# Kernel tuning notes

Measured on AMD Instinct MI355X. Metric: run time of the kernel, lower is better.

The kernel has to match this reference:

```python
import jax, jax.numpy as jnp
import numpy as np

D = 128           # embed_dim
NUM_LAYERS = 2
N_CLASSES = 4
OUT_CELL = 64
SPEAKERS = 2
INPUT_DIMS = [768, 74, 35]
B, T = 32, 60


def setup_inputs() -> dict:
    key = jax.random.key(0)
    ks = jax.random.split(key, 24)
    inp = {}
    inp['x0'] = jax.random.normal(ks[0], (B, T, INPUT_DIMS[0]), jnp.float32)
    inp['x1'] = jax.random.normal(ks[1], (B, T, INPUT_DIMS[1]), jnp.float32)
    inp['x2'] = jax.random.normal(ks[2], (B, T, INPUT_DIMS[2]), jnp.float32)
    inp['smask'] = jax.random.normal(ks[3], (B, T, SPEAKERS), jnp.float32)  # argmax -> speaker ids
    # modality projections
    for i, d in enumerate(INPUT_DIMS):
        inp[f'Wp{i}'] = jax.random.normal(ks[4 + i], (d, D), jnp.float32) / np.float32(np.sqrt(d))
        inp[f'bp{i}'] = jnp.zeros((D,), jnp.float32)
    # shared PositionEmbedding (ModuleList([m]*3) shares params)
    inp['freq_emb'] = jax.random.normal(ks[7], (SPEAKERS, D), jnp.float32) * 0.1
    inp['phase_emb'] = jax.random.normal(ks[8], (SPEAKERS, D), jnp.float32)
    # shared QRNNCell (ModuleList([cell]*num_layers) shares params)
    inp['U_x'] = jnp.linalg.qr(jax.random.normal(ks[9], (D, D), jnp.float32))[0]
    inp['U_h'] = jnp.linalg.qr(jax.random.normal(ks[10], (D, D), jnp.float32))[0]
    inp['Lambda'] = jnp.float32(0.5)
    # QMeasurement kernel (real/imag parts of D measurement vectors)
    inp['kernel_r'] = jnp.eye(D, dtype=jnp.float32) + 0.05 * jax.random.normal(ks[11], (D, D), jnp.float32)
    inp['kernel_i'] = 0.05 * jax.random.normal(ks[12], (D, D), jnp.float32)
    # SimpleNet fc_out
    inp['W1'] = jax.random.normal(ks[13], (D, OUT_CELL), jnp.float32) / np.float32(np.sqrt(D))
    inp['b1'] = jnp.zeros((OUT_CELL,), jnp.float32)
    inp['W2'] = jax.random.normal(ks[14], (OUT_CELL, N_CLASSES), jnp.float32) / np.float32(np.sqrt(OUT_CELL))
    inp['b2'] = jnp.zeros((N_CLASSES,), jnp.float32)
    return inp


def _qmn_forward(x0, x1, x2, smask, Wp0, bp0, Wp1, bp1, Wp2, bp2,
                 freq_emb, phase_emb, U_x, U_h, Lambda,
                 kernel_r, kernel_i, W1, b1, W2, b2):
    xs = [x0, x1, x2]
    Ws = [(Wp0, bp0), (Wp1, bp1), (Wp2, bp2)]
    reps = [jax.nn.relu(x @ W + b) for x, (W, b) in zip(xs, Ws)]           # [B,T,D] each
    # mixture weights: softmax over per-modality L2 norms
    norms = jnp.concatenate([jnp.linalg.norm(r, axis=-1, keepdims=True) for r in reps], axis=-1)
    weights = jax.nn.softmax(norms, axis=-1)                               # [B,T,M]
    # shared phase embedding: phase = t * freq[speaker] + phase[speaker]
    ids = jnp.argmax(smask, axis=-1)                                       # [B,T] int
    pos = jnp.arange(T, dtype=jnp.float32)[None, :, None]                  # [1,T,1]
    phase = pos * freq_emb[ids] + phase_emb[ids]                           # [B,T,D]
    cosp, sinp = jnp.cos(phase), jnp.sin(phase)
    # mixed density matrices rho = sum_m w_m |v_m><v_m|
    rho_r = jnp.zeros((B, T, D, D), jnp.float32)
    rho_i = jnp.zeros((B, T, D, D), jnp.float32)
    for m, r in enumerate(reps):
        a = r / jnp.maximum(jnp.linalg.norm(r, axis=-1, keepdims=True), 1e-12)
        pr = a * cosp                                                       # real amplitude
        pi = a * sinp                                                       # imag amplitude
        w = weights[..., m][..., None, None]
        rho_r = rho_r + w * (jnp.einsum('btm,btn->btmn', pr, pr) + jnp.einsum('btm,btn->btmn', pi, pi))
        rho_i = rho_i + w * (jnp.einsum('btm,btn->btmn', pi, pr) - jnp.einsum('btm,btn->btmn', pr, pi))
    # time-major for scan
    sr = jnp.transpose(rho_r, (1, 0, 2, 3))                                # [T,B,D,D]
    si = jnp.transpose(rho_i, (1, 0, 2, 3))

    def cell(h, x):
        hr, hi = h
        xr, xi = x
        Xr = jnp.einsum('mp,bpq,nq->bmn', U_x, xr, U_x)
        Xi = jnp.einsum('mp,bpq,nq->bmn', U_x, xi, U_x)
        Hr = jnp.einsum('mp,bpq,nq->bmn', U_h, hr, U_h)
        Hi = jnp.einsum('mp,bpq,nq->bmn', U_h, hi, U_h)
        nr = Lambda * Hr + (1.0 - Lambda) * Xr
        ni = Lambda * Hi + (1.0 - Lambda) * Xi
        return (nr, ni), (nr, ni)

    h0 = (jnp.broadcast_to(jnp.eye(D, dtype=jnp.float32) / D, (B, D, D)),
          jnp.zeros((B, D, D), jnp.float32))
    for _ in range(NUM_LAYERS):  # same shared cell params each layer
        _, (sr, si) = jax.lax.scan(cell, h0, (sr, si))
    # QMeasurement: p_k = Re(v_k^dag rho v_k), unit-norm complex measurement vectors
    nrm = jnp.sqrt(jnp.sum(kernel_r**2 + kernel_i**2, axis=1, keepdims=True))
    vr = kernel_r / jnp.maximum(nrm, 1e-12)                                # [K,D], K=D
    vi = kernel_i / jnp.maximum(nrm, 1e-12)
    probs = (jnp.einsum('tbmn,km,kn->tbk', sr, vr, vr)
             + jnp.einsum('tbmn,km,kn->tbk', sr, vi, vi)
             - jnp.einsum('tbmn,km,kn->tbk', si, vr, vi)
             + jnp.einsum('tbmn,km,kn->tbk', si, vi, vr))                  # [T,B,D]
    # SimpleNet (dropout = identity at inference)
    hid = jax.nn.relu(probs @ W1 + b1)
    out = jnp.tanh(hid @ W2 + b2)                                          # [T,B,C]
    out = jnp.transpose(out, (1, 0, 2))                                    # [B,T,C]
    return jax.nn.log_softmax(out, axis=2)


def reference(x0, x1, x2, smask, Wp0, bp0, Wp1, bp1, Wp2, bp2,
              freq_emb, phase_emb, U_x, U_h, Lambda,
              kernel_r, kernel_i, W1, b1, W2, b2):
    return _qmn_forward(x0, x1, x2, smask, Wp0, bp0, Wp1, bp1, Wp2, bp2,
                        freq_emb, phase_emb, U_x, U_h, Lambda,
                        kernel_r, kernel_i, W1, b1, W2, b2)
```

## Files before the change

### kernel.cpp

```cpp
#include <hip/hip_runtime.h>


#define DB 32
#define DT 60
#define DD 128
#define BT (DB*DT)
#define SP 136

typedef unsigned short ushort_t;
typedef __attribute__((ext_vector_type(8))) __bf16 bf16x8;
typedef __attribute__((ext_vector_type(8))) unsigned short ushort8_t;
typedef __attribute__((ext_vector_type(4))) float  float4v;

__device__ __forceinline__ float bf2f(ushort_t u){
  union { unsigned int i; float f; } x; x.i = ((unsigned int)u) << 16; return x.f;
}
__device__ __forceinline__ ushort_t f2bf(float f){
  union { float f; unsigned int i; } x; x.f = f;
  unsigned int lsb = (x.i >> 16) & 1u;
  return (ushort_t)((x.i + 0x7FFFu + lsb) >> 16);
}
__device__ __forceinline__ unsigned int f2bfpk(float a, float b){
#if defined(__gfx950__) && __has_builtin(__builtin_amdgcn_cvt_pk_bf16_f32)
  auto v = __builtin_amdgcn_cvt_pk_bf16_f32(a, b);
  unsigned int r; __builtin_memcpy(&r, &v, 4); return r;
#else
  return (unsigned int)f2bf(a) | ((unsigned int)f2bf(b) << 16);
#endif
}
__device__ __forceinline__ void split2(float v, ushort_t& h, ushort_t& l){
  h = f2bf(v); l = f2bf(v - bf2f(h));
}

template<int RT, int CT, bool ALO, bool BLO>
__device__ __forceinline__ void gemm_t(const ushort_t* Ah, const ushort_t* Al,
                                       const ushort_t* Bh, const ushort_t* Bl,
                                       float4v* acc, int row0, int col0, int gma, int q)
{
  for (int ks = 0; ks < 4; ks++){
    int ko = ks*32 + q*8;
    bf16x8 aF[RT], aL[RT], bF[CT], bL[CT];
    #pragma unroll
    for (int R = 0; R < RT; R++){
      int row = row0 + 16*R + gma;
      aF[R] = *(const bf16x8*)&Ah[row*SP + ko];
      if (ALO) aL[R] = *(const bf16x8*)&Al[row*SP + ko];
    }
    #pragma unroll
    for (int C = 0; C < CT; C++){
      int row = col0 + 16*C + gma;
      bF[C] = *(const bf16x8*)&Bh[row*SP + ko];
      if (BLO) bL[C] = *(const bf16x8*)&Bl[row*SP + ko];
    }
    #pragma unroll
    for (int R = 0; R < RT; R++)
      #pragma unroll
      for (int C = 0; C < CT; C++){
        float4v c = acc[R*CT+C];
        c = __builtin_amdgcn_mfma_f32_16x16x32_bf16(aF[R], bF[C], c, 0, 0, 0);
        if (BLO) c = __builtin_amdgcn_mfma_f32_16x16x32_bf16(aF[R], bL[C], c, 0, 0, 0);
        if (ALO) c = __builtin_amdgcn_mfma_f32_16x16x32_bf16(aL[R], bF[C], c, 0, 0, 0);
        acc[R*CT+C] = c;
      }
  }
}

template<int RT, int CT>
__device__ __forceinline__ void emit_t(const float4v* acc, ushort_t* dst, int stride,
                                       int row0, int col0, int gma, int q){
  #pragma unroll
  for (int R = 0; R < RT; R++)
    #pragma unroll
    for (int C = 0; C < CT; C++){
      int c = col0 + 16*C + gma, r0 = row0 + 16*R + 4*q;
      uint2 o;
      o.x = f2bfpk(acc[R*CT+C][0], acc[R*CT+C][1]);
      o.y = f2bfpk(acc[R*CT+C][2], acc[R*CT+C][3]);
      *(uint2*)&dst[(size_t)c*stride + r0] = o;
    }
}
template<int RT, int CT>
__device__ __forceinline__ void emit_split_t(const float4v* acc, ushort_t* dh, ushort_t* dl, int stride,
                                             int row0, int col0, int gma, int q){
  #pragma unroll
  for (int R = 0; R < RT; R++)
    #pragma unroll
    for (int C = 0; C < CT; C++){
      int c = col0 + 16*C + gma, r0 = row0 + 16*R + 4*q;
      ushort4 hh, ll;
      split2(acc[R*CT+C][0], hh.x, ll.x); split2(acc[R*CT+C][1], hh.y, ll.y);
      split2(acc[R*CT+C][2], hh.z, ll.z); split2(acc[R*CT+C][3], hh.w, ll.w);
      *(ushort4*)&dh[(size_t)c*stride + r0] = hh;
      *(ushort4*)&dl[(size_t)c*stride + r0] = ll;
    }
}
template<int NT>
__device__ __forceinline__ void lds_load_mat(ushort_t* dst, const ushort_t* src, int tid){
  for (int i = tid*8; i < 16384; i += NT*8){
    int r = i >> 7, k = i & 127;
    *(ushort8_t*)&dst[r*SP + k] = *(const ushort8_t*)&src[i];
  }
}
template<int NT>
__device__ __forceinline__ void lds_load_rows16(ushort_t* dst, const ushort_t* src, int tid){
  for (int i = tid*8; i < 2048; i += NT*8){
    int r = i >> 7, k = i & 127;
    *(ushort8_t*)&dst[r*SP + k] = *(const ushort8_t*)&src[i];
  }
}
template<int NT>
__device__ __forceinline__ void lds_load_mat2(ushort_t* d0, const ushort_t* s0,
                                              ushort_t* d1, const ushort_t* s1, int tid){
  constexpr int CH = 16384/(NT*8);
  ushort8_t r0[CH], r1[CH];
  #pragma unroll
  for (int c = 0; c < CH; c++) r0[c] = *(const ushort8_t*)&s0[tid*8 + c*NT*8];
  #pragma unroll
  for (int c = 0; c < CH; c++) r1[c] = *(const ushort8_t*)&s1[tid*8 + c*NT*8];
  #pragma unroll
  for (int c = 0; c < CH; c++){
    int i = tid*8 + c*NT*8; int r = i >> 7, k = i & 127;
    *(ushort8_t*)&d0[r*SP + k] = r0[c];
  }
  #pragma unroll
  for (int c = 0; c < CH; c++){
    int i = tid*8 + c*NT*8; int r = i >> 7, k = i & 127;
    *(ushort8_t*)&d1[r*SP + k] = r1[c];
  }
}
template<int NT>
__device__ __forceinline__ void lds_store_mat(ushort_t* dst, const ushort_t* src, int tid){
  for (int i = tid*8; i < 16384; i += NT*8){
    int r = i >> 7, k = i & 127;
    *(ushort8_t*)&dst[i] = *(const ushort8_t*)&src[r*SP + k];
  }
}

__global__ void k_small(const float* Ux, const float* Uh, const float* kr, const float* ki,
                        const float* Wp0, const float* Wp1, const float* Wp2,
                        const float* x0, const float* x1, const float* x2,
                        ushort_t* UxTh, ushort_t* UxTl, ushort_t* UxH, ushort_t* UxL,
                        float* Vr, float* Vi,
                        ushort_t* PpH, ushort_t* PpL, ushort_t* PTh, ushort_t* PTl,
                        ushort_t* WT0h, ushort_t* WT0l, ushort_t* WT1h, ushort_t* WT1l,
                        ushort_t* WT2h, ushort_t* WT2l,
                        ushort_t* X0h, ushort_t* X0l, ushort_t* X1h, ushort_t* X1l,
                        ushort_t* X2h, ushort_t* X2l){
  int blk = blockIdx.x, d = threadIdx.x;
  if (blk < 128){
    int i = blk;
    float v = Ux[i*DD + d];
    ushort_t h, l; split2(v, h, l);
    UxTh[d*DD + i] = h; UxTl[d*DD + i] = l;
  } else if (blk < 256){
    __shared__ float red[DD];
    int k = blk - 128;
    float r = kr[k*DD+d], im = ki[k*DD+d];
    red[d] = r*r + im*im;
    __syncthreads();
    for (int s = 64; s > 0; s >>= 1){ if (d < s) red[d] += red[d+s]; __syncthreads(); }
    float nrm = fmaxf(sqrtf(red[0]), 1e-12f);
    Vr[k*DD+d] = r/nrm; Vi[k*DD+d] = im/nrm;
  } else if (blk < 384){
    int i = blk - 256;
    float v = Uh[i*DD + d];
    ushort_t h, l; split2(v, h, l);
    PpH[i*DD + d] = h;  PpL[i*DD + d] = l;
    PTh[d*DD + i] = h;  PTl[d*DD + i] = l;
  } else if (blk < 512){
    int dd2 = blk - 384;
    ushort_t h, l;
    for (int k = d; k < 768; k += 128){
      split2(Wp0[(size_t)k*DD + dd2], h, l);
      WT0h[(size_t)dd2*768 + k] = h; WT0l[(size_t)dd2*768 + k] = l;
    }
    { float v = (d < 74) ? Wp1[(size_t)d*DD + dd2] : 0.f;
      split2(v, h, l); WT1h[dd2*128 + d] = h; WT1l[dd2*128 + d] = l; }
    { float v = (d < 35) ? Wp2[(size_t)d*DD + dd2] : 0.f;
      split2(v, h, l); WT2h[dd2*128 + d] = h; WT2l[dd2*128 + d] = l; }
    { split2(Ux[(size_t)dd2*DD + d], h, l);
      UxH[dd2*DD + d] = h; UxL[dd2*DD + d] = l; }
  } else {
    int bt = blk - 512;
    ushort_t h, l;
    const float* r0 = x0 + (size_t)bt*768;
    #pragma unroll
    for (int j = 0; j < 6; j++){
      split2(r0[j*128 + d], h, l);
      X0h[(size_t)bt*768 + j*128 + d] = h;
      X0l[(size_t)bt*768 + j*128 + d] = l;
    }
    float v1 = (d < 74) ? x1[(size_t)bt*74 + d] : 0.f;
    split2(v1, h, l);
    X1h[(size_t)bt*128 + d] = h; X1l[(size_t)bt*128 + d] = l;
    float v2 = (d < 35) ? x2[(size_t)bt*35 + d] : 0.f;
    split2(v2, h, l);
    X2h[(size_t)bt*128 + d] = h; X2l[(size_t)bt*128 + d] = l;
  }
}

__global__ __launch_bounds__(512,1) void k_proj(
    const ushort_t* X0h, const ushort_t* X0l, const ushort_t* X1h, const ushort_t* X1l,
    const ushort_t* X2h, const ushort_t* X2l,
    const ushort_t* WT0h, const ushort_t* WT0l, const ushort_t* WT1h, const ushort_t* WT1l,
    const ushort_t* WT2h, const ushort_t* WT2l,
    const float* bp1, const float* bp2,
    float* Rpart, float* Reps)
{
  __shared__ ushort_t Ah[128*SP], Al[128*SP], Bh[128*SP], Bl[128*SP];
  int blk = blockIdx.x;
  int m, tile, ch;
  if (blk < 90){ m = 0; tile = blk/6; ch = blk%6; }
  else if (blk < 105){ m = 1; tile = blk-90; ch = 0; }
  else { m = 2; tile = blk-105; ch = 0; }
  int bt0 = tile*128;
  int tid = threadIdx.x;
  int w = tid >> 6, lane = tid & 63, gma = lane & 15, q = lane >> 4;
  int row0 = 32*(w >> 1), col0 = 64*(w & 1);
  const ushort_t* Wh_ = (m==0)? WT0h : (m==1)? WT1h : WT2h;
  const ushort_t* Wl_ = (m==0)? WT0l : (m==1)? WT1l : WT2l;
  const ushort_t* Xh_ = (m==0)? X0h : (m==1)? X1h : X2h;
  const ushort_t* Xl_ = (m==0)? X0l : (m==1)? X1l : X2l;
  int KX = (m==0)? 768 : 128;
  for (int i = tid*8; i < 16384; i += 4096){
    int r = i >> 7, k = i & 127;
    *(ushort8_t*)&Ah[r*SP + k] = *(const ushort8_t*)&Wh_[(size_t)r*KX + ch*128 + k];
    *(ushort8_t*)&Al[r*SP + k] = *(const ushort8_t*)&Wl_[(size_t)r*KX + ch*128 + k];
    *(ushort8_t*)&Bh[r*SP + k] = *(const ushort8_t*)&Xh_[(size_t)(bt0+r)*KX + ch*128 + k];
    *(ushort8_t*)&Bl[r*SP + k] = *(const ushort8_t*)&Xl_[(size_t)(bt0+r)*KX + ch*128 + k];
  }
  __syncthreads();
  float4v acc[8];
  #pragma unroll
  for (int i = 0; i < 8; i++) acc[i] = (float4v){0.f,0.f,0.f,0.f};
  gemm_t<2,4,true,true>(Ah, Al, Bh, Bl, acc, row0, col0, gma, q);
  if (m == 0){
    #pragma unroll
    for (int R = 0; R < 2; R++)
      #pragma unroll
      for (int C = 0; C < 4; C++){
        int c = col0 + 16*C + gma, r0 = row0 + 16*R + 4*q;
        float4 o;
        o.x = acc[R*4+C][0]; o.y = acc[R*4+C][1];
        o.z = acc[R*4+C][2]; o.w = acc[R*4+C][3];
        *(float4*)&Rpart[((size_t)ch*BT + bt0 + c)*128 + r0] = o;
      }
  } else {
    const float* bp = (m==1)? bp1 : bp2;
    #pragma unroll
    for (int R = 0; R < 2; R++){
      int r0 = row0 + 16*R + 4*q;
      float4 bv = *(const float4*)&bp[r0];
      #pragma unroll
      for (int C = 0; C < 4; C++){
        int c = col0 + 16*C + gma;
        float4v a = acc[R*4+C];
        float4 o;
        o.x = fmaxf(a[0]+bv.x, 0.f); o.y = fmaxf(a[1]+bv.y, 0.f);
        o.z = fmaxf(a[2]+bv.z, 0.f); o.w = fmaxf(a[3]+bv.w, 0.f);
        *(float4*)&Reps[(size_t)(bt0 + c)*384 + m*128 + r0] = o;
      }
    }
  }
}

__global__ __launch_bounds__(128) void k_mix(const float* Rpart, const float* Reps,
    const float* bp0, const float* smask,
    const float* freq, const float* phem, ushort_t* PsH, ushort_t* PsL, float* Wgt)
{
  __shared__ float part[2][3];
  int bt = blockIdx.x; int t = bt % DT;
  int d = threadIdx.x;
  float r0v = bp0[d];
  #pragma unroll
  for (int ch = 0; ch < 6; ch++)
    r0v += Rpart[((size_t)ch*BT + bt)*128 + d];
  r0v = fmaxf(r0v, 0.f);
  float r1v = Reps[(size_t)bt*384 + 128 + d];
  float r2v = Reps[(size_t)bt*384 + 256 + d];
  float s0 = r0v*r0v, s1 = r1v*r1v, s2 = r2v*r2v;
  #pragma unroll
  for (int off = 1; off < 64; off <<= 1){
    s0 += __shfl_xor(s0, off, 64);
    s1 += __shfl_xor(s1, off, 64);
    s2 += __shfl_xor(s2, off, 64);
  }
  int wv = d >> 6;
  if ((d & 63) == 0){ part[wv][0] = s0; part[wv][1] = s1; part[wv][2] = s2; }
  __syncthreads();
  float n0 = sqrtf(part[0][0] + part[1][0]);
  float n1 = sqrtf(part[0][1] + part[1][1]);
  float n2 = sqrtf(part[0][2] + part[1][2]);
  float mx = fmaxf(n0, fmaxf(n1, n2));
  float e0 = expf(n0-mx), e1 = expf(n1-mx), e2 = expf(n2-mx);
  float einv = 1.f/(e0+e1+e2);
  if (d < 3) Wgt[bt*3+d] = (d==0?e0:(d==1?e1:e2))*einv;
  float sm0 = smask[bt*2], sm1 = smask[bt*2+1];
  int id = (sm1 > sm0) ? 1 : 0;
  float ph = (float)t * freq[id*DD+d] + phem[id*DD+d];
  float cp = cosf(ph), sp = sinf(ph);
  float a0 = r0v / fmaxf(n0, 1e-12f);
  float a1 = r1v / fmaxf(n1, 1e-12f);
  float a2 = r2v / fmaxf(n2, 1e-12f);
  ushort_t h, l;
  split2(a0*cp, h, l); PsH[((size_t)0*BT + bt)*DD + d] = h; PsL[((size_t)0*BT + bt)*DD + d] = l;
  split2(a1*cp, h, l); PsH[((size_t)1*BT + bt)*DD + d] = h; PsL[((size_t)1*BT + bt)*DD + d] = l;
  split2(a2*cp, h, l); PsH[((size_t)2*BT + bt)*DD + d] = h; PsL[((size_t)2*BT + bt)*DD + d] = l;
  split2(a0*sp, h, l); PsH[((size_t)3*BT + bt)*DD + d] = h; PsL[((size_t)3*BT + bt)*DD + d] = l;
  split2(a1*sp, h, l); PsH[((size_t)4*BT + bt)*DD + d] = h; PsL[((size_t)4*BT + bt)*DD + d] = l;
  split2(a2*sp, h, l); PsH[((size_t)5*BT + bt)*DD + d] = h; PsL[((size_t)5*BT + bt)*DD + d] = l;
}

__global__ __launch_bounds__(512,1) void k_qtrans(const ushort_t* UxH, const ushort_t* UxL,
                                                  const ushort_t* PsH, const ushort_t* PsL,
                                                  ushort_t* Qb){
  __shared__ ushort_t Ah[128*SP], Al[128*SP], Bh[128*SP], Bl[128*SP];
  int blk = blockIdx.x;
  int tid = threadIdx.x;
  int w = tid >> 6, lane = tid & 63, gma = lane & 15, q = lane >> 4;
  int row0 = 32*(w >> 1), col0 = 64*(w & 1);
  size_t rbase = (size_t)blk*128*128;
  lds_load_mat<512>(Ah, UxH, tid);
  lds_load_mat<512>(Al, UxL, tid);
  lds_load_mat<512>(Bh, PsH + rbase, tid);
  lds_load_mat<512>(Bl, PsL + rbase, tid);
  __syncthreads();
  float4v acc[8];
  #pragma unroll
  for (int i = 0; i < 8; i++) acc[i] = (float4v){0.f,0.f,0.f,0.f};
  gemm_t<2,4,true,true>(Ah, Al, Bh, Bl, acc, row0, col0, gma, q);
  emit_t<2,4>(acc, Qb + rbase, 128, row0, col0, gma, q);
}

__global__ __launch_bounds__(256,2) void k_pow2v2(ushort_t* PpH, ushort_t* PpL,
                                                  ushort_t* PTh, ushort_t* PTl, int s){
  __shared__ ushort_t Ah[128*SP], Al[128*SP], Bh[16*SP], Bl[16*SP];
  int blk = blockIdx.x;
  int which = blk >> 3, sl = blk & 7;
  size_t src = (size_t)(s-1)*16384, dst = (size_t)s*16384;
  int tid = threadIdx.x;
  int w = tid >> 6, lane = tid & 63, gma = lane & 15, q = lane >> 4;
  int row0 = 32*w;
  int gcol0 = sl*16;
  const ushort_t *A_h, *A_l, *B_h, *B_l; ushort_t *D_h, *D_l;
  if (which == 0){ A_h = PTh+src; A_l = PTl+src; B_h = PpH+src; B_l = PpL+src;
                   D_h = PpH+dst; D_l = PpL+dst; }
  else           { A_h = PpH+src; A_l = PpL+src; B_h = PTh+src; B_l = PTl+src;
                   D_h = PTh+dst; D_l = PTl+dst; }
  lds_load_mat<256>(Ah, A_h, tid);
  lds_load_mat<256>(Al, A_l, tid);
  lds_load_rows16<256>(Bh, B_h + (size_t)gcol0*128, tid);
  lds_load_rows16<256>(Bl, B_l + (size_t)gcol0*128, tid);
  __syncthreads();
  float4v acc[2];
  acc[0] = (float4v){0.f,0.f,0.f,0.f};
  acc[1] = (float4v){0.f,0.f,0.f,0.f};
  gemm_t<2,1,true,true>(Ah, Al, Bh, Bl, acc, row0, 0, gma, q);
  emit_split_t<2,1>(acc, D_h, D_l, 128, row0, gcol0, gma, q);
}

__global__ __launch_bounds__(512,1) void k_gchain(const ushort_t* PpH, const ushort_t* PpL,
                                                  const ushort_t* PTh, const ushort_t* PTl,
                                                  ushort_t* GTh, ushort_t* GTl){
  __shared__ ushort_t Ah[128*SP], Al[128*SP], Bh[128*SP], Bl[128*SP];
  int t = blockIdx.x;
  int tid = threadIdx.x;
  int w = tid >> 6, lane = tid & 63, gma = lane & 15, q = lane >> 4;
  int row0 = 32*(w >> 1), col0 = 64*(w & 1);
  size_t gslot = (size_t)t * 16384;
  if (t == 0){
    for (int i = tid*4; i < 16384; i += 2048){
      int r = i >> 7, k = i & 127;
      ushort4 zz; zz.x = zz.y = zz.z = zz.w = 0;
      *(ushort4*)&GTl[gslot + i] = zz;
      ushort4 oh;
      oh.x = (r == (k+0)) ? (ushort_t)0x3F80 : (ushort_t)0;
      oh.y = (r == (k+1)) ? (ushort_t)0x3F80 : (ushort_t)0;
      oh.z = (r == (k+2)) ? (ushort_t)0x3F80 : (ushort_t)0;
      oh.w = (r == (k+3)) ? (ushort_t)0x3F80 : (ushort_t)0;
      *(ushort4*)&GTh[gslot + i] = oh;
    }
    return;
  }
  int b0 = __ffs(t) - 1;
  int rem = t & ~(1 << b0);
  if (rem == 0){
    size_t ps = (size_t)b0 * 16384;
    for (int i = tid*4; i < 16384; i += 2048){
      *(ushort4*)&GTh[gslot + i] = *(const ushort4*)&PTh[ps + i];
      *(ushort4*)&GTl[gslot + i] = *(const ushort4*)&PTl[ps + i];
    }
    return;
  }
  lds_load_mat<512>(Ah, PpH + (size_t)b0*16384, tid);
  lds_load_mat<512>(Al, PpL + (size_t)b0*16384, tid);
  while (rem){
    int k = __ffs(rem) - 1;
    rem &= ~(1 << k);
    lds_load_mat<512>(Bh, PTh + (size_t)k*16384, tid);
    lds_load_mat<512>(Bl, PTl + (size_t)k*16384, tid);
    __syncthreads();
    float4v acc[8];
    #pragma unroll
    for (int i = 0; i < 8; i++) acc[i] = (float4v){0.f,0.f,0.f,0.f};
    if (rem){
      gemm_t<2,4,true,true>(Bh, Bl, Ah, Al, acc, row0, col0, gma, q);
      __syncthreads();
      emit_split_t<2,4>(acc, Ah, Al, SP, row0, col0, gma, q);
      __syncthreads();
    } else {
      gemm_t<2,4,true,true>(Ah, Al, Bh, Bl, acc, row0, col0, gma, q);
      emit_split_t<2,4>(acc, GTh + gslot, GTl + gslot, 128, row0, col0, gma, q);
    }
  }
}

__global__ __launch_bounds__(256,1) void k_precompMW(const ushort_t* GTh, const ushort_t* GTl,
                                                     const ushort_t* UxTh, const ushort_t* UxTl,
                                                     const float* Vr, const float* Vi,
                                                     ushort_t* Mh, ushort_t* Wh){
  __shared__ ushort_t Bh[128*SP], Bl[128*SP], Ah[128*SP], Al[128*SP];
  int blk = blockIdx.x;
  int tid = threadIdx.x;
  int w = tid >> 6, lane = tid & 63, gma = lane & 15, q = lane >> 4;
  int row0 = 64*(w >> 1), col0 = 64*(w & 1);
  if (blk < 60){
    int t = blk;
    lds_load_mat<256>(Bh, GTh + (size_t)t*16384, tid);
    lds_load_mat<256>(Bl, GTl + (size_t)t*16384, tid);
    lds_load_mat<256>(Ah, UxTh, tid);
    lds_load_mat<256>(Al, UxTl, tid);
    __syncthreads();
    float4v acc[16];
    #pragma unroll
    for (int i = 0; i < 16; i++) acc[i] = (float4v){0.f,0.f,0.f,0.f};
    gemm_t<4,4,true,true>(Ah, Al, Bh, Bl, acc, row0, col0, gma, q);
    __syncthreads();
    emit_split_t<4,4>(acc, Ah, Al, SP, row0, col0, gma, q);
    __syncthreads();
    #pragma unroll
    for (int i = 0; i < 16; i++) acc[i] = (float4v){0.f,0.f,0.f,0.f};
    gemm_t<4,4,true,true>(Bh, Bl, Ah, Al, acc, row0, col0, gma, q);
    #pragma unroll
    for (int R = 0; R < 4; R++)
      #pragma unroll
      for (int C = 0; C < 4; C++){
        int c = col0 + 16*C + gma, r0 = row0 + 16*R + 4*q;
        uint2 o;
        o.x = f2bfpk(acc[R*4+C][0], acc[R*4+C][1]);
        o.y = f2bfpk(acc[R*4+C][2], acc[R*4+C][3]);
        *(uint2*)&Mh[(size_t)t*16384 + c*128 + r0] = o;
      }
  } else {
    int bx = blk - 60;
    int t = bx >> 1, which = bx & 1;
    lds_load_mat<256>(Ah, GTh + (size_t)t*16384, tid);
    lds_load_mat<256>(Al, GTl + (size_t)t*16384, tid);
    const float* V = which ? Vi : Vr;
    for (int i = tid; i < 16384; i += 256){
      int r = i >> 7, k = i & 127;
      ushort_t h, l; split2(V[i], h, l);
      Bh[r*SP + k] = h; Bl[r*SP + k] = l;
    }
    __syncthreads();
    float4v acc[16];
    #pragma unroll
    for (int i = 0; i < 16; i++) acc[i] = (float4v){0.f,0.f,0.f,0.f};
    gemm_t<4,4,true,true>(Ah, Al, Bh, Bl, acc, row0, col0, gma, q);
    #pragma unroll
    for (int R = 0; R < 4; R++)
      #pragma unroll
      for (int C = 0; C < 4; C++){
        int c = col0 + 16*C + gma, r0 = row0 + 16*R + 4*q;
        uint2 o;
        o.x = f2bfpk(acc[R*4+C][0], acc[R*4+C][1]);
        o.y = f2bfpk(acc[R*4+C][2], acc[R*4+C][3]);
        *(uint2*)&Wh[(size_t)bx*16384 + c*128 + r0] = o;
      }
  }
}

__global__ __launch_bounds__(512,1) void k_vtrans(const ushort_t* GTh, const ushort_t* Qb, ushort_t* At){
  __shared__ ushort_t Ah[128*SP];
  __shared__ ushort_t Bs[192*SP];
  int t = blockIdx.x;
  int tid = threadIdx.x;
  int w = tid >> 6, lane = tid & 63, gma = lane & 15, q = lane >> 4;
  int row0 = (w & 3)*32, col0 = (w >> 2)*96;
  lds_load_mat<512>(Ah, GTh + (size_t)t*16384, tid);
  for (int i = tid*8; i < 192*128; i += 4096){
    int m = i >> 7, k = i & 127;
    int j = m >> 5, b = m & 31;
    *(ushort8_t*)&Bs[m*SP + k] =
      *(const ushort8_t*)&Qb[((size_t)(j*BT) + b*DT + t)*DD + k];
  }
  __syncthreads();
  float4v acc[12];
  #pragma unroll
  for (int i = 0; i < 12; i++) acc[i] = (float4v){0.f,0.f,0.f,0.f};
  gemm_t<2,6,false,false>(Ah, Ah, Bs, Bs, acc, row0, col0, gma, q);
  emit_t<2,6>(acc, At + (size_t)t*24576, 128, row0, col0, gma, q);
}

__global__ __launch_bounds__(256) void k_zbuild(ushort_t* S, const ushort_t* At,
                                                const float* Wgt, const float* lamp){
  __shared__ ushort_t As[2][6*DD];
  __shared__ float wl[2][3];
  int blk = blockIdx.x;
  int b = blk >> 5, sl2 = blk & 31;
  int tid = threadIdx.x;
  int r = sl2*4 + (tid >> 6);
  int c = (tid*2) & 127;
  float lam = lamp[0];
  float z0 = 0.f, z1 = 0.f;
  size_t off = (size_t)sl2*512 + tid*2;
  ushort4 pre;
  float wpre = 0.f;
  int jj0 = 0, n0 = 0;
  if (tid < 192){
    int i = tid*4;
    jj0 = i >> 7; n0 = i & 127;
    pre = *(const ushort4*)&At[(size_t)(jj0*32 + b)*128 + n0];
  }
  if (tid < 3) wpre = Wgt[(b*DT)*3 + tid];
  for (int t = 0; t < DT; t++){
    int cur = t & 1;
    if (tid < 192) *(ushort4*)&As[cur][tid*4] = pre;
    if (tid < 3) wl[cur][tid] = wpre;
    __syncthreads();
    if (t+1 < DT){
      if (tid < 192)
        pre = *(const ushort4*)&At[(size_t)(t+1)*24576 + (size_t)(jj0*32 + b)*128 + n0];
      if (tid < 3) wpre = Wgt[(b*DT + t+1)*3 + tid];
    }
    float ar[6];
    #pragma unroll
    for (int jj = 0; jj < 6; jj++) ar[jj] = bf2f(As[cur][jj*128 + r]);
    float w0 = wl[cur][0], w1 = wl[cur][1], w2 = wl[cur][2];
    float cb[6];
    cb[0] = w0*(ar[0]+ar[3]); cb[1] = w1*(ar[1]+ar[4]); cb[2] = w2*(ar[2]+ar[5]);
    cb[3] = w0*(ar[3]-ar[0]); cb[4] = w1*(ar[4]-ar[1]); cb[5] = w2*(ar[5]-ar[2]);
    float y0 = 0.f, y1 = 0.f;
    #pragma unroll
    for (int jj = 0; jj < 6; jj++){
      unsigned int a2 = *(const unsigned int*)&As[cur][jj*128 + c];
      float w_ = cb[jj];
      y0 += w_*bf2f((ushort_t)(a2 & 0xFFFF));
      y1 += w_*bf2f((ushort_t)(a2 >> 16));
    }
    z0 = lam*z0 + y0; z1 = lam*z1 + y1;
    *(unsigned int*)&S[((size_t)(t*32 + b))*16384 + off] = f2bfpk(z0, z1);
  }
}

__global__ __launch_bounds__(512,2) void k_conjmid(ushort_t* S, const ushort_t* Mh,
                                                   const float* lamp){
  __shared__ ushort_t Bh[128*SP], Zs[128*SP];
  int raw = blockIdx.x;
  int g = raw & 7, t = raw >> 3;
  int tid = threadIdx.x;
  int w = tid >> 6, lane = tid & 63, gma = lane & 15, q = lane >> 4;
  int row0 = 32*(w >> 1), col0 = 64*(w & 1);
  size_t slot0 = (size_t)(t*32 + g*4) * 16384;
  lds_load_mat2<512>(Zs, S + slot0, Bh, Mh + (size_t)t*16384, tid);
  __syncthreads();
  float lam = lamp[0];
  float oml = 1.f - lam;
  float ct = powf(lam, (float)(t+1)) / 128.f;
  for (int ib = 0; ib < 4; ib++){
    size_t slot = slot0 + (size_t)ib*16384;
    ushort8_t znext[4];
    if (ib < 3){
      #pragma unroll
      for (int c = 0; c < 4; c++)
        znext[c] = *(const ushort8_t*)&S[slot + 16384 + tid*8 + c*4096];
    }
    float4v acc[8];
    #pragma unroll
    for (int i = 0; i < 8; i++) acc[i] = (float4v){0.f,0.f,0.f,0.f};
    gemm_t<2,4,false,false>(Zs, Zs, Bh, Bh, acc, row0, col0, gma, q);
    __syncthreads();
    emit_t<2,4>(acc, Zs, SP, row0, col0, gma, q);
    __syncthreads();
    #pragma unroll
    for (int i = 0; i < 8; i++) acc[i] = (float4v){0.f,0.f,0.f,0.f};
    gemm_t<2,4,false,false>(Zs, Zs, Bh, Bh, acc, row0, col0, gma, q);
    __syncthreads();
    #pragma unroll
    for (int R = 0; R < 2; R++)
      #pragma unroll
      for (int C = 0; C < 4; C++){
        int c = col0 + 16*C + gma, r0 = row0 + 16*R + 4*q;
        float v0 = oml*acc[R*4+C][0] + ((c == r0+0) ? ct : 0.f);
        float v1 = oml*acc[R*4+C][1] + ((c == r0+1) ? ct : 0.f);
        float v2 = oml*acc[R*4+C][2] + ((c == r0+2) ? ct : 0.f);
        float v3 = oml*acc[R*4+C][3] + ((c == r0+3) ? ct : 0.f);
        uint2 o; o.x = f2bfpk(v0, v1); o.y = f2bfpk(v2, v3);
        *(uint2*)&Zs[(size_t)c*SP + r0] = o;
      }
    __syncthreads();
    lds_store_mat<512>(S + slot, Zs, tid);
    if (ib < 3){
      __syncthreads();
      #pragma unroll
      for (int c = 0; c < 4; c++){
        int i = tid*8 + c*4096;
        int r = i >> 7, k = i & 127;
        *(ushort8_t*)&Zs[r*SP + k] = znext[c];
      }
      __syncthreads();
    }
  }
}

__device__ __forceinline__ void prefix_ph2(uint2& buf, bool doload,
                                           const ushort_t* Snext, ushort_t* Scur,
                                           float* a, float lam){
  uint2 u = buf;
  if (doload) buf = *(const uint2*)Snext;
  a[0] = lam*a[0] + bf2f((ushort_t)(u.x & 0xFFFF));
  a[1] = lam*a[1] + bf2f((ushort_t)(u.x >> 16));
  a[2] = lam*a[2] + bf2f((ushort_t)(u.y & 0xFFFF));
  a[3] = lam*a[3] + bf2f((ushort_t)(u.y >> 16));
  uint2 o;
  o.x = f2bfpk(a[0], a[1]); o.y = f2bfpk(a[2], a[3]);
  *(uint2*)Scur = o;
}
__global__ __launch_bounds__(128) void k_prefix(ushort_t* S, const float* lamp){
  int blk = blockIdx.x;
  int chain = blk >> 5, slab = blk & 31;
  int tid = threadIdx.x;
  size_t off = (size_t)slab*512 + tid*4;
  float lam = lamp[0];
  float a[4];
  #pragma unroll
  for (int i = 0; i < 4; i++) a[i] = 0.f;
  size_t addr = (size_t)chain*16384 + off;
  const size_t step = (size_t)32*16384;
  uint2 b0 = *(const uint2*)&S[addr];
  uint2 b1 = *(const uint2*)&S[addr + step];
  uint2 b2 = *(const uint2*)&S[addr + 2*step];
  uint2 b3 = *(const uint2*)&S[addr + 3*step];
  uint2 b4 = *(const uint2*)&S[addr + 4*step];
  uint2 b5 = *(const uint2*)&S[addr + 5*step];
  for (int t = 0; t < DT; t += 6){
    prefix_ph2(b0, t+6  < DT, &S[addr + 6*step], &S[addr], a, lam); addr += step;
    prefix_ph2(b1, t+7  < DT, &S[addr + 6*step], &S[addr], a, lam); addr += step;
    prefix_ph2(b2, t+8  < DT, &S[addr + 6*step], &S[addr], a, lam); addr += step;
    prefix_ph2(b3, t+9  < DT, &S[addr + 6*step], &S[addr], a, lam); addr += step;
    prefix_ph2(b4, t+10 < DT, &S[addr + 6*step], &S[addr], a, lam); addr += step;
    prefix_ph2(b5, t+11 < DT, &S[addr + 6*step], &S[addr], a, lam); addr += step;
  }
}

__global__ __launch_bounds__(512,2) void k_meas(const ushort_t* S, const ushort_t* Wh,
                                                const float* lamp, float* Probs){
  __shared__ ushort_t Vs[128*SP], Cs[128*SP];
  __shared__ float Pd[64];
  int raw = blockIdx.x;
  int g = raw & 7;
  int h = (raw >> 3) & 1;
  int t = raw >> 4;
  int tid = threadIdx.x;
  int w = tid >> 6, lane = tid & 63, gma = lane & 15, q = lane >> 4;
  int row0 = 16*(w >> 1);
  int col0 = 64*(w & 1);
  size_t wbase = (size_t)(t*2) * 16384;
  size_t slot0 = (size_t)(t*32 + g*4) * 16384;
  ushort8_t creg[4], vreg[4];
  #pragma unroll
  for (int c = 0; c < 4; c++)
    creg[c] = *(const ushort8_t*)&S[slot0 + tid*8 + c*4096];
  #pragma unroll
  for (int c = 0; c < 4; c++){
    int i = tid*8 + c*4096;
    int r = i >> 7, k = i & 127;
    size_t gsrc = wbase + ((r < 64) ? 0 : 16384) + (size_t)(64*h + (r & 63))*128 + k;
    vreg[c] = *(const ushort8_t*)&Wh[gsrc];
  }
  if (tid < 64) Pd[tid] = 0.f;
  #pragma unroll
  for (int c = 0; c < 4; c++){
    int i = tid*8 + c*4096;
    int r = i >> 7, k = i & 127;
    *(ushort8_t*)&Cs[r*SP + k] = creg[c];
    *(ushort8_t*)&Vs[r*SP + k] = vreg[c];
  }
  __syncthreads();
  float lam = lamp[0];
  float ct = powf(lam, (float)(t+1)) / 128.f;
  for (int ib = 0; ib < 4; ib++){
    if (ib < 3){
      size_t snx = slot0 + (size_t)(ib+1)*16384;
      #pragma unroll
      for (int c = 0; c < 4; c++)
        creg[c] = *(const ushort8_t*)&S[snx + tid*8 + c*4096];
    }
    float4v acc[8];
    #pragma unroll
    for (int i = 0; i < 8; i++) acc[i] = (float4v){0.f,0.f,0.f,0.f};
    #pragma unroll
    for (int ks = 0; ks < 4; ks++){
      int ko = ks*32 + q*8;
      bf16x8 aF0 = *(const bf16x8*)&Vs[(row0 + gma)*SP + ko];
      bf16x8 aF1 = *(const bf16x8*)&Vs[(row0 + 64 + gma)*SP + ko];
      bf16x8 bF[4];
      #pragma unroll
      for (int C = 0; C < 4; C++)
        bF[C] = *(const bf16x8*)&Cs[(col0 + 16*C + gma)*SP + ko];
      #pragma unroll
      for (int C = 0; C < 4; C++){
        acc[C]   = __builtin_amdgcn_mfma_f32_16x16x32_bf16(aF0, bF[C], acc[C],   0, 0, 0);
        acc[4+C] = __builtin_amdgcn_mfma_f32_16x16x32_bf16(aF1, bF[C], acc[4+C], 0, 0, 0);
      }
    }
    #pragma unroll
    for (int j = 0; j < 4; j++){
      int kr = row0 + 4*q + j;
      float s = 0.f;
      #pragma unroll
      for (int C = 0; C < 4; C++){
        int m = col0 + 16*C + gma;
        float w0 = bf2f(Vs[kr*SP + m]);
        float w1 = bf2f(Vs[(kr + 64)*SP + m]);
        s += acc[C][j]*(w0 + w1) + acc[4+C][j]*(w1 - w0);
      }
      #pragma unroll
      for (int off = 1; off < 16; off <<= 1)
        s += __shfl_xor(s, off, 64);
      if (gma == 0) atomicAdd(&Pd[kr], s);
    }
    __syncthreads();
    if (tid < 64){
      Probs[(size_t)(t*32 + g*4 + ib)*DD + 64*h + tid] = (1.f - lam)*Pd[tid] + ct;
      Pd[tid] = 0.f;
    }
    if (ib < 3){
      #pragma unroll
      for (int c = 0; c < 4; c++){
        int i = tid*8 + c*4096;
        int r = i >> 7, k = i & 127;
        *(ushort8_t*)&Cs[r*SP + k] = creg[c];
      }
    }
    __syncthreads();
  }
}

__global__ __launch_bounds__(64) void k_head(const float* Probs, const float* W1, const float* b1,
                        const float* W2, const float* b2, float* out)
{
  __shared__ float ps[DD];
  __shared__ float hid[64];
  __shared__ float ov[4];
  int tb = blockIdx.x;
  int tid = threadIdx.x;
  ps[tid] = Probs[(size_t)tb*DD + tid];
  ps[tid+64] = Probs[(size_t)tb*DD + 64 + tid];
  __syncthreads();
  float acc = b1[tid];
  for (int dd = 0; dd < DD; dd++) acc += ps[dd]*W1[dd*64 + tid];
  hid[tid] = fmaxf(acc, 0.f);
  __syncthreads();
  if (tid < 4){
    float o = b2[tid];
    for (int j = 0; j < 64; j++) o += hid[j]*W2[j*4 + tid];
    ov[tid] = tanhf(o);
  }
  __syncthreads();
  if (tid == 0){
    float m = fmaxf(fmaxf(ov[0],ov[1]), fmaxf(ov[2],ov[3]));
    float lse = logf(expf(ov[0]-m)+expf(ov[1]-m)+expf(ov[2]-m)+expf(ov[3]-m));
    int t = tb >> 5, b = tb & 31;
    float* o = out + ((size_t)(b*DT + t))*4;
    o[0] = ov[0]-m-lse; o[1] = ov[1]-m-lse;
    o[2] = ov[2]-m-lse; o[3] = ov[3]-m-lse;
  }
}

extern "C" void kernel_launch(void* const* d_in, const int* in_sizes, int n_in,
                              void* d_out, int out_size, void* d_ws, size_t ws_size,
                              hipStream_t stream)
{
  const float* x0    = (const float*)d_in[0];
  const float* x1    = (const float*)d_in[1];
  const float* x2    = (const float*)d_in[2];
  const float* smask = (const float*)d_in[3];
  const float* Wp0   = (const float*)d_in[4];
  const float* bp0   = (const float*)d_in[5];
  const float* Wp1   = (const float*)d_in[6];
  const float* bp1   = (const float*)d_in[7];
  const float* Wp2   = (const float*)d_in[8];
  const float* bp2   = (const float*)d_in[9];
  const float* freq  = (const float*)d_in[10];
  const float* phem  = (const float*)d_in[11];
  const float* Ux    = (const float*)d_in[12];
  const float* Uh    = (const float*)d_in[13];
  const float* lamp  = (const float*)d_in[14];
  const float* kr    = (const float*)d_in[15];
  const float* ki    = (const float*)d_in[16];
  const float* W1    = (const float*)d_in[17];
  const float* b1    = (const float*)d_in[18];
  const float* W2    = (const float*)d_in[19];
  const float* b2    = (const float*)d_in[20];

  char* ws = (char*)d_ws;
  auto alignup = [](size_t x){ return (x + 255) & ~(size_t)255; };
  size_t off = 0;
  ushort_t* S   = (ushort_t*)(ws + off); off = alignup(off + (size_t)1920*16384*sizeof(ushort_t));
  ushort_t* Qb  = (ushort_t*)(ws + off); off = alignup(off + (size_t)6*BT*DD*sizeof(ushort_t));
  float* Rpart  = (float*)(ws + off);    off = alignup(off + (size_t)6*BT*DD*sizeof(float));
  float* Reps   = (float*)(ws + off);    off = alignup(off + (size_t)BT*384*sizeof(float));
  ushort_t* PsH = (ushort_t*)(ws + off); off = alignup(off + (size_t)6*BT*DD*sizeof(ushort_t));
  ushort_t* PsL = (ushort_t*)(ws + off); off = alignup(off + (size_t)6*BT*DD*sizeof(ushort_t));
  ushort_t* X0h = (ushort_t*)(ws + off); off = alignup(off + (size_t)BT*768*sizeof(ushort_t));
  ushort_t* X0l = (ushort_t*)(ws + off); off = alignup(off + (size_t)BT*768*sizeof(ushort_t));
  ushort_t* X1h = (ushort_t*)(ws + off); off = alignup(off + (size_t)BT*128*sizeof(ushort_t));
  ushort_t* X1l = (ushort_t*)(ws + off); off = alignup(off + (size_t)BT*128*sizeof(ushort_t));
  ushort_t* X2h = (ushort_t*)(ws + off); off = alignup(off + (size_t)BT*128*sizeof(ushort_t));
  ushort_t* X2l = (ushort_t*)(ws + off); off = alignup(off + (size_t)BT*128*sizeof(ushort_t));
  float* Wgt    = (float*)(ws + off);    off = alignup(off + (size_t)BT*3*sizeof(float));
  float* Vr     = (float*)(ws + off);    off = alignup(off + (size_t)DD*DD*sizeof(float));
  float* Vi     = (float*)(ws + off);    off = alignup(off + (size_t)DD*DD*sizeof(float));
  ushort_t* UxTh = (ushort_t*)(ws + off); off = alignup(off + (size_t)DD*DD*sizeof(ushort_t));
  ushort_t* UxTl = (ushort_t*)(ws + off); off = alignup(off + (size_t)DD*DD*sizeof(ushort_t));
  ushort_t* UxH = (ushort_t*)(ws + off); off = alignup(off + (size_t)DD*DD*sizeof(ushort_t));
  ushort_t* UxL = (ushort_t*)(ws + off); off = alignup(off + (size_t)DD*DD*sizeof(ushort_t));
  float* Probs  = (float*)(ws + off);    off = alignup(off + (size_t)BT*DD*sizeof(float));
  ushort_t* PpH = (ushort_t*)(ws + off); off = alignup(off + (size_t)6*16384*sizeof(ushort_t));
  ushort_t* PpL = (ushort_t*)(ws + off); off = alignup(off + (size_t)6*16384*sizeof(ushort_t));
  ushort_t* PTh = (ushort_t*)(ws + off); off = alignup(off + (size_t)6*16384*sizeof(ushort_t));
  ushort_t* PTl = (ushort_t*)(ws + off); off = alignup(off + (size_t)6*16384*sizeof(ushort_t));
  ushort_t* Mh  = (ushort_t*)(ws + off); off = alignup(off + (size_t)60*16384*sizeof(ushort_t));
  ushort_t* Wmh = (ushort_t*)(ws + off); off = alignup(off + (size_t)120*16384*sizeof(ushort_t));
  ushort_t* GTh = (ushort_t*)(ws + off); off = alignup(off + (size_t)60*16384*sizeof(ushort_t));
  ushort_t* GTl = (ushort_t*)(ws + off); off = alignup(off + (size_t)60*16384*sizeof(ushort_t));
  ushort_t* At  = (ushort_t*)(ws + off); off = alignup(off + (size_t)60*24576*sizeof(ushort_t));
  ushort_t* WT0h = (ushort_t*)(ws + off); off = alignup(off + (size_t)128*768*sizeof(ushort_t));
  ushort_t* WT0l = (ushort_t*)(ws + off); off = alignup(off + (size_t)128*768*sizeof(ushort_t));
  ushort_t* WT1h = (ushort_t*)(ws + off); off = alignup(off + (size_t)128*128*sizeof(ushort_t));
  ushort_t* WT1l = (ushort_t*)(ws + off); off = alignup(off + (size_t)128*128*sizeof(ushort_t));
  ushort_t* WT2h = (ushort_t*)(ws + off); off = alignup(off + (size_t)128*128*sizeof(ushort_t));
  ushort_t* WT2l = (ushort_t*)(ws + off); off = alignup(off + (size_t)128*128*sizeof(ushort_t));
  (void)ws_size; (void)in_sizes; (void)n_in; (void)out_size;

  k_small<<<512 + BT, 128, 0, stream>>>(Ux, Uh, kr, ki, Wp0, Wp1, Wp2, x0, x1, x2,
                                        UxTh, UxTl, UxH, UxL, Vr, Vi,
                                        PpH, PpL, PTh, PTl,
                                        WT0h, WT0l, WT1h, WT1l, WT2h, WT2l,
                                        X0h, X0l, X1h, X1l, X2h, X2l);
  k_proj<<<120, 512, 0, stream>>>(X0h, X0l, X1h, X1l, X2h, X2l,
                                  WT0h, WT0l, WT1h, WT1l, WT2h, WT2l,
                                  bp1, bp2, Rpart, Reps);
  k_mix<<<BT, 128, 0, stream>>>(Rpart, Reps, bp0, smask, freq, phem, PsH, PsL, Wgt);
  k_qtrans<<<90, 512, 0, stream>>>(UxH, UxL, PsH, PsL, Qb);
  for (int s = 1; s <= 5; s++)
    k_pow2v2<<<16, 256, 0, stream>>>(PpH, PpL, PTh, PTl, s);
  k_gchain<<<60, 512, 0, stream>>>(PpH, PpL, PTh, PTl, GTh, GTl);
  k_precompMW<<<180, 256, 0, stream>>>(GTh, GTl, UxTh, UxTl, Vr, Vi, Mh, Wmh);
  k_vtrans<<<60, 512, 0, stream>>>(GTh, Qb, At);
  k_zbuild<<<1024, 256, 0, stream>>>(S, At, Wgt, lamp);
  k_conjmid<<<480, 512, 0, stream>>>(S, Mh, lamp);
  k_prefix<<<1024, 128, 0, stream>>>(S, lamp);
  k_meas<<<960, 512, 0, stream>>>(S, Wmh, lamp, Probs);
  k_head<<<BT, 64, 0, stream>>>(Probs, W1, b1, W2, b2, (float*)d_out);
}
```

Baseline: 310.8 us.

## Fold pow2 steps into proj/qtrans launches and merge precompMW with vtrans

The first two matrix-power steps (s=1, s=2) now run as extra blocks of the k_proj and k_qtrans launches instead of as separate small kernels. k_precompMW and k_vtrans are merged into a single 512-thread kernel with a shared LDS buffer, and the 256-thread paths leave half the threads idle. The aim is fewer kernel launches and less serialization of tiny 16-block kernels, at the cost of lower per-block thread use for the precompMW part and larger LDS footprints for the pow2 blocks.

```diff
diff --git a/kernel.cpp b/kernel.cpp
--- a/kernel.cpp
+++ b/kernel.cpp
@@ -133,6 +133,36 @@
   for (int i = tid*8; i < 16384; i += NT*8){
     int r = i >> 7, k = i & 127;
     *(ushort8_t*)&dst[i] = *(const ushort8_t*)&src[r*SP + k];
+  }
+}
+
+__device__ __forceinline__ void pow2_body(int blk2, int s,
+    ushort_t* PpH, ushort_t* PpL, ushort_t* PTh, ushort_t* PTl,
+    int tid, ushort_t* Ah, ushort_t* Al, ushort_t* Bh, ushort_t* Bl)
+{
+  int which = blk2 >> 3, sl = blk2 & 7;
+  size_t src = (size_t)(s-1)*16384, dst = (size_t)s*16384;
+  int gcol0 = sl*16;
+  const ushort_t *A_h, *A_l, *B_h, *B_l; ushort_t *D_h, *D_l;
+  if (which == 0){ A_h = PTh+src; A_l = PTl+src; B_h = PpH+src; B_l = PpL+src;
+                   D_h = PpH+dst; D_l = PpL+dst; }
+  else           { A_h = PpH+src; A_l = PpL+src; B_h = PTh+src; B_l = PTl+src;
+                   D_h = PTh+dst; D_l = PTl+dst; }
+  if (tid < 256){
+    lds_load_mat<256>(Ah, A_h, tid);
+    lds_load_mat<256>(Al, A_l, tid);
+    lds_load_rows16<256>(Bh, B_h + (size_t)gcol0*128, tid);
+    lds_load_rows16<256>(Bl, B_l + (size_t)gcol0*128, tid);
+  }
+  __syncthreads();
+  if (tid < 256){
+    int w = tid >> 6, lane = tid & 63, gma = lane & 15, q = lane >> 4;
+    int row0 = 32*w;
+    float4v acc[2];
+    acc[0] = (float4v){0.f,0.f,0.f,0.f};
+    acc[1] = (float4v){0.f,0.f,0.f,0.f};
+    gemm_t<2,1,true,true>(Ah, Al, Bh, Bl, acc, row0, 0, gma, q);
+    emit_split_t<2,1>(acc, D_h, D_l, 128, row0, gcol0, gma, q);
   }
 }
 
@@ -205,16 +235,21 @@
     const ushort_t* WT0h, const ushort_t* WT0l, const ushort_t* WT1h, const ushort_t* WT1l,
     const ushort_t* WT2h, const ushort_t* WT2l,
     const float* bp1, const float* bp2,
-    float* Rpart, float* Reps)
+    float* Rpart, float* Reps,
+    ushort_t* PpH, ushort_t* PpL, ushort_t* PTh, ushort_t* PTl)
 {
   __shared__ ushort_t Ah[128*SP], Al[128*SP], Bh[128*SP], Bl[128*SP];
   int blk = blockIdx.x;
+  int tid = threadIdx.x;
+  if (blk >= 120){
+    pow2_body(blk - 120, 1, PpH, PpL, PTh, PTl, tid, Ah, Al, Bh, Bl);
+    return;
+  }
   int m, tile, ch;
   if (blk < 90){ m = 0; tile = blk/6; ch = blk%6; }
   else if (blk < 105){ m = 1; tile = blk-90; ch = 0; }
   else { m = 2; tile = blk-105; ch = 0; }
   int bt0 = tile*128;
-  int tid = threadIdx.x;
   int w = tid >> 6, lane = tid & 63, gma = lane & 15, q = lane >> 4;
   int row0 = 32*(w >> 1), col0 = 64*(w & 1);
   const ushort_t* Wh_ = (m==0)? WT0h : (m==1)? WT1h : WT2h;
@@ -313,10 +348,16 @@
 
 __global__ __launch_bounds__(512,1) void k_qtrans(const ushort_t* UxH, const ushort_t* UxL,
                                                   const ushort_t* PsH, const ushort_t* PsL,
-                                                  ushort_t* Qb){
+                                                  ushort_t* Qb,
+                                                  ushort_t* PpH, ushort_t* PpL,
+                                                  ushort_t* PTh, ushort_t* PTl){
   __shared__ ushort_t Ah[128*SP], Al[128*SP], Bh[128*SP], Bl[128*SP];
   int blk = blockIdx.x;
   int tid = threadIdx.x;
+  if (blk >= 90){
+    pow2_body(blk - 90, 2, PpH, PpL, PTh, PTl, tid, Ah, Al, Bh, Bl);
+    return;
+  }
   int w = tid >> 6, lane = tid & 63, gma = lane & 15, q = lane >> 4;
   int row0 = 32*(w >> 1), col0 = 64*(w & 1);
   size_t rbase = (size_t)blk*128*128;
@@ -415,91 +456,107 @@
   }
 }
 
-__global__ __launch_bounds__(256,1) void k_precompMW(const ushort_t* GTh, const ushort_t* GTl,
-                                                     const ushort_t* UxTh, const ushort_t* UxTl,
-                                                     const float* Vr, const float* Vi,
-                                                     ushort_t* Mh, ushort_t* Wh){
-  __shared__ ushort_t Bh[128*SP], Bl[128*SP], Ah[128*SP], Al[128*SP];
+__global__ __launch_bounds__(512,1) void k_mwvt(
+    const ushort_t* GTh, const ushort_t* GTl,
+    const ushort_t* UxTh, const ushort_t* UxTl,
+    const float* Vr, const float* Vi,
+    const ushort_t* Qb,
+    ushort_t* Mh, ushort_t* Wh, ushort_t* At)
+{
+  __shared__ ushort_t LBUF[4*128*SP];
   int blk = blockIdx.x;
   int tid = threadIdx.x;
-  int w = tid >> 6, lane = tid & 63, gma = lane & 15, q = lane >> 4;
-  int row0 = 64*(w >> 1), col0 = 64*(w & 1);
-  if (blk < 60){
-    int t = blk;
-    lds_load_mat<256>(Bh, GTh + (size_t)t*16384, tid);
-    lds_load_mat<256>(Bl, GTl + (size_t)t*16384, tid);
-    lds_load_mat<256>(Ah, UxTh, tid);
-    lds_load_mat<256>(Al, UxTl, tid);
+  if (blk < 180){
+    ushort_t* Bh = LBUF;
+    ushort_t* Bl = LBUF + 128*SP;
+    ushort_t* Ah = LBUF + 2*128*SP;
+    ushort_t* Al = LBUF + 3*128*SP;
+    int w = tid >> 6, lane = tid & 63, gma = lane & 15, q = lane >> 4;
+    int row0 = 64*(w >> 1), col0 = 64*(w & 1);
+    if (blk < 60){
+      int t = blk;
+      if (tid < 256){
+        lds_load_mat<256>(Bh, GTh + (size_t)t*16384, tid);
+        lds_load_mat<256>(Bl, GTl + (size_t)t*16384, tid);
+        lds_load_mat<256>(Ah, UxTh, tid);
+        lds_load_mat<256>(Al, UxTl, tid);
+      }
+      __syncthreads();
+      float4v acc[16];
+      if (tid < 256){
+        #pragma unroll
+        for (int i = 0; i < 16; i++) acc[i] = (float4v){0.f,0.f,0.f,0.f};
+        gemm_t<4,4,true,true>(Ah, Al, Bh, Bl, acc, row0, col0, gma, q);
+      }
+      __syncthreads();
+      if (tid < 256) emit_split_t<4,4>(acc, Ah, Al, SP, row0, col0, gma, q);
+      __syncthreads();
+      if (tid < 256){
+        #pragma unroll
+        for (int i = 0; i < 16; i++) acc[i] = (float4v){0.f,0.f,0.f,0.f};
+        gemm_t<4,4,true,true>(Bh, Bl, Ah, Al, acc, row0, col0, gma, q);
+        #pragma unroll
+        for (int R = 0; R < 4; R++)
+          #pragma unroll
+          for (int C = 0; C < 4; C++){
+            int c = col0 + 16*C + gma, r0 = row0 + 16*R + 4*q;
+            uint2 o;
+            o.x = f2bfpk(acc[R*4+C][0], acc[R*4+C][1]);
+            o.y = f2bfpk(acc[R*4+C][2], acc[R*4+C][3]);
+            *(uint2*)&Mh[(size_t)t*16384 + c*128 + r0] = o;
+          }
+      }
+    } else {
+      int bx = blk - 60;
+      int t = bx >> 1, which = bx & 1;
+      if (tid < 256){
+        lds_load_mat<256>(Ah, GTh + (size_t)t*16384, tid);
+        lds_load_mat<256>(Al, GTl + (size_t)t*16384, tid);
+        const float* V = which ? Vi : Vr;
+        for (int i = tid; i < 16384; i += 256){
+          int r = i >> 7, k = i & 127;
+          ushort_t h, l; split2(V[i], h, l);
+          Bh[r*SP + k] = h; Bl[r*SP + k] = l;
+        }
+      }
+      __syncthreads();
+      if (tid < 256){
+        float4v acc[16];
+        #pragma unroll
+        for (int i = 0; i < 16; i++) acc[i] = (float4v){0.f,0.f,0.f,0.f};
+        gemm_t<4,4,true,true>(Ah, Al, Bh, Bl, acc, row0, col0, gma, q);
+        #pragma unroll
+        for (int R = 0; R < 4; R++)
+          #pragma unroll
+          for (int C = 0; C < 4; C++){
+            int c = col0 + 16*C + gma, r0 = row0 + 16*R + 4*q;
+            uint2 o;
+            o.x = f2bfpk(acc[R*4+C][0], acc[R*4+C][1]);
+            o.y = f2bfpk(acc[R*4+C][2], acc[R*4+C][3]);
+            *(uint2*)&Wh[(size_t)bx*16384 + c*128 + r0] = o;
+          }
+      }
+    }
+  } else {
+    ushort_t* Ah = LBUF;
+    ushort_t* Bs = LBUF + 128*SP;
+    int t = blk - 180;
+    int w = tid >> 6, lane = tid & 63, gma = lane & 15, q = lane >> 4;
+    int row0 = (w & 3)*32, col0 = (w >> 2)*96;
+    lds_load_mat<512>(Ah, GTh + (size_t)t*16384, tid);
+    for (int i = tid*8; i < 192*128; i += 4096){
+      int m = i >> 7, k = i & 127;
+      int j = m >> 5, b = m & 31;
+      *(ushort8_t*)&Bs[m*SP + k] =
+        *(const ushort8_t*)&Qb[((size_t)(j*BT) + b*DT + t)*DD + k];
+    }
     __syncthreads();
-    float4v acc[16];
-    #pragma unroll
-    for (int i = 0; i < 16; i++) acc[i] = (float4v){0.f,0.f,0.f,0.f};
-    gemm_t<4,4,true,true>(Ah, Al, Bh, Bl, acc, row0, col0, gma, q);
-    __syncthreads();
-    emit_split_t<4,4>(acc, Ah, Al, SP, row0, col0, gma, q);
-    __syncthreads();
-    #pragma unroll
-    for (int i = 0; i < 16; i++) acc[i] = (float4v){0.f,0.f,0.f,0.f};
-    gemm_t<4,4,true,true>(Bh, Bl, Ah, Al, acc, row0, col0, gma, q);
-    #pragma unroll
-    for (int R = 0; R < 4; R++)
-      #pragma unroll
-      for (int C = 0; C < 4; C++){
-        int c = col0 + 16*C + gma, r0 = row0 + 16*R + 4*q;
-        uint2 o;
-        o.x = f2bfpk(acc[R*4+C][0], acc[R*4+C][1]);
-        o.y = f2bfpk(acc[R*4+C][2], acc[R*4+C][3]);
-        *(uint2*)&Mh[(size_t)t*16384 + c*128 + r0] = o;
-      }
-  } else {
-    int bx = blk - 60;
-    int t = bx >> 1, which = bx & 1;
-    lds_load_mat<256>(Ah, GTh + (size_t)t*16384, tid);
-    lds_load_mat<256>(Al, GTl + (size_t)t*16384, tid);
-    const float* V = which ? Vi : Vr;
-    for (int i = tid; i < 16384; i += 256){
-      int r = i >> 7, k = i & 127;
-      ushort_t h, l; split2(V[i], h, l);
-      Bh[r*SP + k] = h; Bl[r*SP + k] = l;
-    }
-    __syncthreads();
-    float4v acc[16];
-    #pragma unroll
-    for (int i = 0; i < 16; i++) acc[i] = (float4v){0.f,0.f,0.f,0.f};
-    gemm_t<4,4,true,true>(Ah, Al, Bh, Bl, acc, row0, col0, gma, q);
-    #pragma unroll
-    for (int R = 0; R < 4; R++)
-      #pragma unroll
-      for (int C = 0; C < 4; C++){
-        int c = col0 + 16*C + gma, r0 = row0 + 16*R + 4*q;
-        uint2 o;
-        o.x = f2bfpk(acc[R*4+C][0], acc[R*4+C][1]);
-        o.y = f2bfpk(acc[R*4+C][2], acc[R*4+C][3]);
-        *(uint2*)&Wh[(size_t)bx*16384 + c*128 + r0] = o;
-      }
-  }
-}
-
-__global__ __launch_bounds__(512,1) void k_vtrans(const ushort_t* GTh, const ushort_t* Qb, ushort_t* At){
-  __shared__ ushort_t Ah[128*SP];
-  __shared__ ushort_t Bs[192*SP];
-  int t = blockIdx.x;
-  int tid = threadIdx.x;
-  int w = tid >> 6, lane = tid & 63, gma = lane & 15, q = lane >> 4;
-  int row0 = (w & 3)*32, col0 = (w >> 2)*96;
-  lds_load_mat<512>(Ah, GTh + (size_t)t*16384, tid);
-  for (int i = tid*8; i < 192*128; i += 4096){
-    int m = i >> 7, k = i & 127;
-    int j = m >> 5, b = m & 31;
-    *(ushort8_t*)&Bs[m*SP + k] =
-      *(const ushort8_t*)&Qb[((size_t)(j*BT) + b*DT + t)*DD + k];
-  }
-  __syncthreads();
-  float4v acc[12];
-  #pragma unroll
-  for (int i = 0; i < 12; i++) acc[i] = (float4v){0.f,0.f,0.f,0.f};
-  gemm_t<2,6,false,false>(Ah, Ah, Bs, Bs, acc, row0, col0, gma, q);
-  emit_t<2,6>(acc, At + (size_t)t*24576, 128, row0, col0, gma, q);
+    float4v acc[12];
+    #pragma unroll
+    for (int i = 0; i < 12; i++) acc[i] = (float4v){0.f,0.f,0.f,0.f};
+    gemm_t<2,6,false,false>(Ah, Ah, Bs, Bs, acc, row0, col0, gma, q);
+    emit_t<2,6>(acc, At + (size_t)t*24576, 128, row0, col0, gma, q);
+  }
 }
 
 __global__ __launch_bounds__(256) void k_zbuild(ushort_t* S, const ushort_t* At,
@@ -849,16 +906,15 @@
                                         PpH, PpL, PTh, PTl,
                                         WT0h, WT0l, WT1h, WT1l, WT2h, WT2l,
                                         X0h, X0l, X1h, X1l, X2h, X2l);
-  k_proj<<<120, 512, 0, stream>>>(X0h, X0l, X1h, X1l, X2h, X2l,
+  k_proj<<<136, 512, 0, stream>>>(X0h, X0l, X1h, X1l, X2h, X2l,
                                   WT0h, WT0l, WT1h, WT1l, WT2h, WT2l,
-                                  bp1, bp2, Rpart, Reps);
+                                  bp1, bp2, Rpart, Reps, PpH, PpL, PTh, PTl);
   k_mix<<<BT, 128, 0, stream>>>(Rpart, Reps, bp0, smask, freq, phem, PsH, PsL, Wgt);
-  k_qtrans<<<90, 512, 0, stream>>>(UxH, UxL, PsH, PsL, Qb);
-  for (int s = 1; s <= 5; s++)
+  k_qtrans<<<106, 512, 0, stream>>>(UxH, UxL, PsH, PsL, Qb, PpH, PpL, PTh, PTl);
+  for (int s = 3; s <= 5; s++)
     k_pow2v2<<<16, 256, 0, stream>>>(PpH, PpL, PTh, PTl, s);
   k_gchain<<<60, 512, 0, stream>>>(PpH, PpL, PTh, PTl, GTh, GTl);
-  k_precompMW<<<180, 256, 0, stream>>>(GTh, GTl, UxTh, UxTl, Vr, Vi, Mh, Wmh);
-  k_vtrans<<<60, 512, 0, stream>>>(GTh, Qb, At);
+  k_mwvt<<<240, 512, 0, stream>>>(GTh, GTl, UxTh, UxTl, Vr, Vi, Qb, Mh, Wmh, At);
   k_zbuild<<<1024, 256, 0, stream>>>(S, At, Wgt, lamp);
   k_conjmid<<<480, 512, 0, stream>>>(S, Mh, lamp);
   k_prefix<<<1024, 128, 0, stream>>>(S, lamp);
```

Measured after the change: 296.2 us. 4.7% less time.
